# Kernel tuning notes

Measured on AMD Instinct MI355X. Metric: run time of the kernel, lower is better.

Reference implementation:

```python
import jax, jax.numpy as jnp
import numpy as np
from jax.scipy.special import ndtri

NUM_BITS = 4
BLOCK_SIZE = 64
OUT_F, IN_F = 4096, 4096


def _nf_table(num_bits=NUM_BITS):
    # Faithful to NFQuantizer.create_normal_map (asymmetric branch)
    offset = 0.9677083
    variations = 2 ** num_bits
    v1 = ndtri(jnp.linspace(offset, 0.5, variations // 2 + 1, dtype=jnp.float32)[:-1])
    v3 = -ndtri(jnp.linspace(offset, 0.5, variations // 2, dtype=jnp.float32)[:-1])
    v = jnp.concatenate([v1, jnp.zeros((1,), jnp.float32), v3])
    v = jnp.sort(v)
    return v / v.max()


def setup_inputs() -> dict:
    key = jax.random.key(0)
    k1, k2, k3, k4, k5 = jax.random.split(key, 5)
    x = jax.random.normal(k1, (8192, IN_F), dtype=jnp.float32)
    qweight = jax.random.randint(k2, (IN_F * OUT_F // 2, 1), 0, 256, dtype=jnp.int32)
    absmax = jax.random.uniform(k3, (IN_F * OUT_F // BLOCK_SIZE, 1), dtype=jnp.float32) * 0.1 + 1e-3
    lora_A = jax.random.normal(k4, (64, IN_F), dtype=jnp.float32) * 0.02
    lora_B = jax.random.normal(k5, (OUT_F, 64), dtype=jnp.float32) * 0.02
    return {"x": x, "qweight": qweight, "absmax": absmax, "lora_A": lora_A, "lora_B": lora_B}


def reference(x, qweight, absmax, lora_A, lora_B):
    table = _nf_table()
    q = qweight[:, 0]
    # dequantize_block: low nibble first (i=0), then high nibble (i=1)
    idx = jnp.stack([q & 0xF, (q >> NUM_BITS) & 0xF], axis=-1)  # [Q, 2]
    w = table[idx].reshape(-1, BLOCK_SIZE) * absmax             # [n_blocks, block_size]
    w = w.reshape(OUT_F, IN_F)
    dense = x @ w.T
    lora = (x @ lora_A.T) @ lora_B.T
    return dense + lora
```

## Files before the change

### kernel.cpp

```cpp
#include <hip/hip_runtime.h>

#define IN_F 4096
#define OUT_F 4096
#define M_ROWS 8192
#define GK 4096

typedef float  floatx4 __attribute__((ext_vector_type(4)));
typedef short  shortx8 __attribute__((ext_vector_type(8)));

__device__ __forceinline__ unsigned short f2bf(float f) {
    unsigned int u = __float_as_uint(f);
    u = (u + 0x7FFFu + ((u >> 16) & 1u)) >> 16;
    return (unsigned short)u;
}

__constant__ float NF4_TAB[16] = {
    -1.0f, -0.6961928009986877f, -0.5250730514526367f, -0.39491748809814453f,
    -0.28444138169288635f, -0.18477343022823334f, -0.09105003625154495f, 0.0f,
    0.07958029955625534f, 0.16093020141124725f, 0.2461123913526535f, 0.33791524171829224f,
    0.44070982933044434f, 0.5626170039176941f, 0.7229568362236023f, 1.0f
};

__device__ __forceinline__ void gll16(const void* g, void* l) {
    __builtin_amdgcn_global_load_lds(
        (const __attribute__((address_space(1))) void*)g,
        (__attribute__((address_space(3))) void*)l, 16, 0, 0);
}

__global__ __launch_bounds__(256) void prep(
    const float* __restrict__ A, const float* __restrict__ Bm,
    const float* __restrict__ x,
    short* __restrict__ At, short* __restrict__ Bb, short* __restrict__ Xb)
{
    __shared__ float tile[64][65];
    const int b = blockIdx.x;
    const int t = threadIdx.x;

    if (b < 64) {
        const int ib = b * 64;
        const int r = t >> 2, c0 = (t & 3) * 16;
        #pragma unroll
        for (int k = 0; k < 4; ++k) {
            float4 v = *(const float4*)(A + (size_t)r * IN_F + ib + c0 + k * 4);
            tile[r][c0 + k * 4 + 0] = v.x;
            tile[r][c0 + k * 4 + 1] = v.y;
            tile[r][c0 + k * 4 + 2] = v.z;
            tile[r][c0 + k * 4 + 3] = v.w;
        }
        __syncthreads();
        const int i = t >> 2, r0 = (t & 3) * 16;
        union { unsigned short u[8]; int4 v; } p0, p1;
        #pragma unroll
        for (int k = 0; k < 8; ++k) p0.u[k] = f2bf(tile[r0 + k][i]);
        #pragma unroll
        for (int k = 0; k < 8; ++k) p1.u[k] = f2bf(tile[r0 + 8 + k][i]);
        *(int4*)(At + (size_t)(ib + i) * 64 + r0)     = p0.v;
        *(int4*)(At + (size_t)(ib + i) * 64 + r0 + 8) = p1.v;
    } else if (b < 192) {
        const size_t i = ((size_t)(b - 64) * 256 + t) * 8;
        float4 a = *(const float4*)(Bm + i);
        float4 c = *(const float4*)(Bm + i + 4);
        union { unsigned short u[8]; int4 v; } p;
        p.u[0] = f2bf(a.x); p.u[1] = f2bf(a.y); p.u[2] = f2bf(a.z); p.u[3] = f2bf(a.w);
        p.u[4] = f2bf(c.x); p.u[5] = f2bf(c.y); p.u[6] = f2bf(c.z); p.u[7] = f2bf(c.w);
        *(int4*)(Bb + i) = p.v;
    } else {
        const size_t i = ((size_t)(b - 192) * 256 + t) * 8;
        float4 a = *(const float4*)(x + i);
        float4 c = *(const float4*)(x + i + 4);
        union { unsigned short u[8]; int4 v; } p;
        p.u[0] = f2bf(a.x); p.u[1] = f2bf(a.y); p.u[2] = f2bf(a.z); p.u[3] = f2bf(a.w);
        p.u[4] = f2bf(c.x); p.u[5] = f2bf(c.y); p.u[6] = f2bf(c.z); p.u[7] = f2bf(c.w);
        *(int4*)(Xb + i) = p.v;
    }
}

#define BM 128
#define BN 128

__global__ __launch_bounds__(256) void lora_weff(
    const short* __restrict__ Bb,
    const short* __restrict__ At,
    const int*   __restrict__ qw,
    const float* __restrict__ absmax,
    short*       __restrict__ W)
{
    __shared__ short As[BM * 32];
    __shared__ short Bs[BN * 32];
    __shared__ float nf4s[16];
    __shared__ float amS[256];

    const int tid  = threadIdx.x;
    const int lane = tid & 63;
    const int wave = tid >> 6;
    const int bn = blockIdx.x * BN;
    const int bm = blockIdx.y * BM;

    if (tid < 16) nf4s[tid] = NF4_TAB[tid];
    amS[tid] = absmax[(size_t)(bm + (tid & 127)) * 64 + (bn >> 6) + (tid >> 7)];

    const int ar = tid >> 2;
    const int ac = ((tid & 3) ^ ((ar >> 1) & 3)) * 8;
    const short* gA0 = Bb + (size_t)(bm + ar) * 64 + ac;
    const short* gA1 = gA0 + (size_t)64 * 64;
    const short* gB0 = At + (size_t)(bn + ar) * 64 + ac;
    const short* gB1 = gB0 + (size_t)64 * 64;
    short* lA0 = As + tid * 8;
    short* lA1 = As + 2048 + tid * 8;
    short* lB0 = Bs + tid * 8;
    short* lB1 = Bs + 2048 + tid * 8;

    const int wm = (wave >> 1) * 64;
    const int wn = (wave & 1) * 64;
    const int fr = lane & 15;
    const int fk_sw = (((lane >> 4) ^ ((fr >> 1) & 3))) * 8;

    floatx4 zero = {0.f, 0.f, 0.f, 0.f};
    floatx4 acc[4][4];
    #pragma unroll
    for (int i = 0; i < 4; ++i)
        #pragma unroll
        for (int j = 0; j < 4; ++j) acc[i][j] = zero;

    #pragma unroll
    for (int kt = 0; kt < 2; ++kt) {
        gll16(gA0, lA0);
        gll16(gA1, lA1);
        gll16(gB0, lB0);
        gll16(gB1, lB1);
        gA0 += 32; gA1 += 32; gB0 += 32; gB1 += 32;
        __syncthreads();

        shortx8 af[4], bfr[4];
        #pragma unroll
        for (int i = 0; i < 4; ++i) {
            af[i]  = *(const shortx8*)&As[(wm + i * 16 + fr) * 32 + fk_sw];
            bfr[i] = *(const shortx8*)&Bs[(wn + i * 16 + fr) * 32 + fk_sw];
        }
        #pragma unroll
        for (int i = 0; i < 4; ++i)
            #pragma unroll
            for (int j = 0; j < 4; ++j)
                acc[i][j] = __builtin_amdgcn_mfma_f32_16x16x32_bf16(
                    af[i], bfr[j], acc[i][j], 0, 0, 0);
        __syncthreads();
    }

    const int row0  = bm + wm + (lane >> 4) * 4;
    const int col0  = bn + wn + fr;
    const int amsel = (wn >> 6) * 128;
    #pragma unroll
    for (int i = 0; i < 4; ++i) {
        #pragma unroll
        for (int rr = 0; rr < 4; ++rr) {
            const int o = row0 + i * 16 + rr;
            const float am = amS[amsel + (o - bm)];
            #pragma unroll
            for (int j = 0; j < 4; ++j) {
                const int ic = col0 + j * 16;
                const size_t flat = (size_t)o * IN_F + ic;
                const int q = qw[flat >> 1];
                const int nib = (fr & 1) ? ((q >> 4) & 15) : (q & 15);
                const unsigned v = f2bf(fmaf(nf4s[nib], am, acc[i][j][rr]));
                const unsigned hi = (unsigned)__shfl_xor((int)v, 1, 64);
                if (!(fr & 1))
                    *(unsigned*)(W + flat) = v | (hi << 16);
            }
        }
    }
}

#define BK 64

__global__ __launch_bounds__(256) void gemm_bt(
    const short* __restrict__ Xb,
    const short* __restrict__ Wb,
    float*       __restrict__ C)
{
    __shared__ short As[BM * BK];
    __shared__ short Bs[BN * BK];

    const int tid  = threadIdx.x;
    const int lane = tid & 63;
    const int wave = tid >> 6;
    const int bn = blockIdx.x * BN;
    const int bm = blockIdx.y * BM;

    const int ar  = tid >> 3;
    const int gc  = (tid & 7) ^ (ar & 7);
    const short* gA = Xb + (size_t)(bm + ar) * GK + gc * 8;
    const short* gB = Wb + (size_t)(bn + ar) * GK + gc * 8;
    short* lA = As + tid * 8;
    short* lB = Bs + tid * 8;

    const int wm = (wave >> 1) * 64;
    const int wn = (wave & 1) * 64;
    const int fr = lane & 15;
    const int qd = lane >> 4;
    const int rsw = fr & 7;

    floatx4 zero = {0.f, 0.f, 0.f, 0.f};
    floatx4 acc[4][4];
    #pragma unroll
    for (int i = 0; i < 4; ++i)
        #pragma unroll
        for (int j = 0; j < 4; ++j) acc[i][j] = zero;

    for (int kt = 0; kt < GK / BK; ++kt) {
        #pragma unroll
        for (int r = 0; r < 4; ++r) {
            gll16(gA + (size_t)r * 32 * GK, lA + r * 2048);
            gll16(gB + (size_t)r * 32 * GK, lB + r * 2048);
        }
        gA += BK; gB += BK;
        __syncthreads();

        #pragma unroll
        for (int ks = 0; ks < 2; ++ks) {
            const int p = ((ks * 4 + qd) ^ rsw) * 8;
            shortx8 af[4], bfr[4];
            #pragma unroll
            for (int i = 0; i < 4; ++i) {
                af[i]  = *(const shortx8*)&As[(wm + i * 16 + fr) * BK + p];
                bfr[i] = *(const shortx8*)&Bs[(wn + i * 16 + fr) * BK + p];
            }
            #pragma unroll
            for (int i = 0; i < 4; ++i)
                #pragma unroll
                for (int j = 0; j < 4; ++j)
                    acc[i][j] = __builtin_amdgcn_mfma_f32_16x16x32_bf16(
                        af[i], bfr[j], acc[i][j], 0, 0, 0);
        }
        __syncthreads();
    }

    const int row0 = bm + wm + qd * 4;
    const int col0 = bn + wn + fr;
    #pragma unroll
    for (int i = 0; i < 4; ++i)
        #pragma unroll
        for (int j = 0; j < 4; ++j) {
            float* cp = C + (size_t)(row0 + i * 16) * OUT_F + col0 + j * 16;
            #pragma unroll
            for (int rr = 0; rr < 4; ++rr)
                cp[(size_t)rr * OUT_F] = acc[i][j][rr];
        }
}

extern "C" void kernel_launch(void* const* d_in, const int* in_sizes, int n_in,
                              void* d_out, int out_size, void* d_ws, size_t ws_size,
                              hipStream_t stream) {
    const float* x  = (const float*)d_in[0];
    const int*   qw = (const int*)d_in[1];
    const float* am = (const float*)d_in[2];
    const float* lA = (const float*)d_in[3];
    const float* lB = (const float*)d_in[4];
    float* out = (float*)d_out;

    short* Weff = (short*)d_ws;
    short* Xb   = (short*)((char*)d_ws + (size_t)OUT_F * IN_F * 2);
    short* At   = (short*)((char*)d_ws + (size_t)(OUT_F * IN_F + M_ROWS * IN_F) * 2);
    short* Bb   = At + (size_t)IN_F * 64;

    prep<<<192 + (M_ROWS * IN_F) / 2048, 256, 0, stream>>>(lA, lB, x, At, Bb, Xb);
    lora_weff<<<dim3(IN_F / 128, OUT_F / 128), 256, 0, stream>>>(Bb, At, qw, am, Weff);
    gemm_bt<<<dim3(OUT_F / BN, M_ROWS / BM), 256, 0, stream>>>(Xb, Weff, out);
}
```

Before: 544.5 us.

## Stage LoRA tile through LDS for coalesced Weff writes; remap GEMM blocks per XCD

The LoRA+dequant epilogue now writes the bf16 LoRA product transposed into shared memory. Each thread then reads one output row segment, dequantizes NF4 weights from prefetched vectorized qweight loads, and writes 16-byte coalesced stores. This replaces scattered per-element qweight loads and the shuffle-based 4-byte stores. Separately, the main GEMM remaps block indices so that blocks landing on each XCD cover a contiguous 2D tile region, improving L2 reuse. The cost is an extra bf16 rounding of the LoRA term before the add and additional LDS traffic.

```diff
diff --git a/kernel.cpp b/kernel.cpp
--- a/kernel.cpp
+++ b/kernel.cpp
@@ -12,6 +12,10 @@
     unsigned int u = __float_as_uint(f);
     u = (u + 0x7FFFu + ((u >> 16) & 1u)) >> 16;
     return (unsigned short)u;
+}
+
+__device__ __forceinline__ float bf2f(unsigned short u) {
+    return __uint_as_float((unsigned)u << 16);
 }
 
 __constant__ float NF4_TAB[16] = {
@@ -85,10 +89,11 @@
     const float* __restrict__ absmax,
     short*       __restrict__ W)
 {
-    __shared__ short As[BM * 32];
-    __shared__ short Bs[BN * 32];
+    __shared__ union SMem {
+        struct { short As[BM * 32]; short Bs[BN * 32]; } mm;
+        short Wt[128 * 136];
+    } sm;
     __shared__ float nf4s[16];
-    __shared__ float amS[256];
 
     const int tid  = threadIdx.x;
     const int lane = tid & 63;
@@ -97,7 +102,15 @@
     const int bm = blockIdx.y * BM;
 
     if (tid < 16) nf4s[tid] = NF4_TAB[tid];
-    amS[tid] = absmax[(size_t)(bm + (tid & 127)) * 64 + (bn >> 6) + (tid >> 7)];
+
+    const int r_o = tid >> 1;
+    const int h   = tid & 1;
+    const int go  = bm + r_o;
+    const int* qbase = qw + (size_t)go * 2048 + (bn >> 1) + h * 32;
+    int4 q4[8];
+    #pragma unroll
+    for (int k = 0; k < 8; ++k) q4[k] = *(const int4*)(qbase + 4 * k);
+    const float am = absmax[(size_t)go * 64 + (bn >> 6) + h];
 
     const int ar = tid >> 2;
     const int ac = ((tid & 3) ^ ((ar >> 1) & 3)) * 8;
@@ -105,14 +118,15 @@
     const short* gA1 = gA0 + (size_t)64 * 64;
     const short* gB0 = At + (size_t)(bn + ar) * 64 + ac;
     const short* gB1 = gB0 + (size_t)64 * 64;
-    short* lA0 = As + tid * 8;
-    short* lA1 = As + 2048 + tid * 8;
-    short* lB0 = Bs + tid * 8;
-    short* lB1 = Bs + 2048 + tid * 8;
+    short* lA0 = sm.mm.As + tid * 8;
+    short* lA1 = sm.mm.As + 2048 + tid * 8;
+    short* lB0 = sm.mm.Bs + tid * 8;
+    short* lB1 = sm.mm.Bs + 2048 + tid * 8;
 
     const int wm = (wave >> 1) * 64;
     const int wn = (wave & 1) * 64;
     const int fr = lane & 15;
+    const int qd = lane >> 4;
     const int fk_sw = (((lane >> 4) ^ ((fr >> 1) & 3))) * 8;
 
     floatx4 zero = {0.f, 0.f, 0.f, 0.f};
@@ -134,8 +148,8 @@
         shortx8 af[4], bfr[4];
         #pragma unroll
         for (int i = 0; i < 4; ++i) {
-            af[i]  = *(const shortx8*)&As[(wm + i * 16 + fr) * 32 + fk_sw];
-            bfr[i] = *(const shortx8*)&Bs[(wn + i * 16 + fr) * 32 + fk_sw];
+            af[i]  = *(const shortx8*)&sm.mm.As[(wm + i * 16 + fr) * 32 + fk_sw];
+            bfr[i] = *(const shortx8*)&sm.mm.Bs[(wn + i * 16 + fr) * 32 + fk_sw];
         }
         #pragma unroll
         for (int i = 0; i < 4; ++i)
@@ -146,27 +160,37 @@
         __syncthreads();
     }
 
-    const int row0  = bm + wm + (lane >> 4) * 4;
-    const int col0  = bn + wn + fr;
-    const int amsel = (wn >> 6) * 128;
     #pragma unroll
     for (int i = 0; i < 4; ++i) {
-        #pragma unroll
-        for (int rr = 0; rr < 4; ++rr) {
-            const int o = row0 + i * 16 + rr;
-            const float am = amS[amsel + (o - bm)];
-            #pragma unroll
-            for (int j = 0; j < 4; ++j) {
-                const int ic = col0 + j * 16;
-                const size_t flat = (size_t)o * IN_F + ic;
-                const int q = qw[flat >> 1];
-                const int nib = (fr & 1) ? ((q >> 4) & 15) : (q & 15);
-                const unsigned v = f2bf(fmaf(nf4s[nib], am, acc[i][j][rr]));
-                const unsigned hi = (unsigned)__shfl_xor((int)v, 1, 64);
-                if (!(fr & 1))
-                    *(unsigned*)(W + flat) = v | (hi << 16);
-            }
-        }
+        const int r0 = wm + i * 16 + qd * 4;
+        #pragma unroll
+        for (int j = 0; j < 4; ++j) {
+            const int c = wn + j * 16 + fr;
+            union { unsigned short u[4]; uint2 v; } p;
+            p.u[0] = f2bf(acc[i][j][0]);
+            p.u[1] = f2bf(acc[i][j][1]);
+            p.u[2] = f2bf(acc[i][j][2]);
+            p.u[3] = f2bf(acc[i][j][3]);
+            *(uint2*)&sm.Wt[c * 136 + r0] = p.v;
+        }
+    }
+    __syncthreads();
+
+    short* out = W + (size_t)go * IN_F + bn + h * 64;
+    #pragma unroll
+    for (int k = 0; k < 8; ++k) {
+        const int qs[4] = { q4[k].x, q4[k].y, q4[k].z, q4[k].w };
+        union { unsigned short u[8]; int4 v; } p;
+        #pragma unroll
+        for (int d = 0; d < 4; ++d) {
+            const int q = qs[d];
+            const int c = h * 64 + k * 8 + d * 2;
+            const float l0 = bf2f((unsigned short)sm.Wt[c * 136 + r_o]);
+            const float l1 = bf2f((unsigned short)sm.Wt[(c + 1) * 136 + r_o]);
+            p.u[2 * d]     = f2bf(fmaf(nf4s[q & 15],        am, l0));
+            p.u[2 * d + 1] = f2bf(fmaf(nf4s[(q >> 4) & 15], am, l1));
+        }
+        *(int4*)(out + k * 8) = p.v;
     }
 }
 
@@ -183,8 +207,14 @@
     const int tid  = threadIdx.x;
     const int lane = tid & 63;
     const int wave = tid >> 6;
-    const int bn = blockIdx.x * BN;
-    const int bm = blockIdx.y * BM;
+
+    const int orig = blockIdx.y * gridDim.x + blockIdx.x;
+    const int xcd  = orig & 7;
+    const int t8   = orig >> 3;
+    const int bxp  = (xcd & 1) * 16 + (t8 & 15);
+    const int byp  = (xcd >> 1) * 16 + (t8 >> 4);
+    const int bn = bxp * BN;
+    const int bm = byp * BM;
 
     const int ar  = tid >> 3;
     const int gc  = (tid & 7) ^ (ar & 7);
```

Measured after the change: 540.5 us. Within noise of the previous version (-0.7%).
